# Kernel optimization log

Measured on AMD Instinct MI355X. Metric: run time of the kernel, lower is better.

Reference implementation:

```python
import jax, jax.numpy as jnp
import numpy as np

ALPHA = 4.0          # spikingjelly default surrogate.Sigmoid(alpha=4.0)
V_TH = 1.0           # IFNode default v_threshold
BN_EPS = 1e-5

@jax.custom_vjp
def spike(x):
    # heaviside forward
    return (x >= 0.0).astype(x.dtype)

def _spike_fwd(x):
    return spike(x), x

def _spike_bwd(x, g):
    s = jax.nn.sigmoid(ALPHA * x)
    return (g * ALPHA * s * (1.0 - s),)

spike.defvjp(_spike_fwd, _spike_bwd)

def if_node(x_seq):
    """Multi-step IF neuron: integrate, threshold, hard reset (v_reset=0),
    detach_reset=True. x_seq: [T, ...] -> spikes [T, ...]."""
    def step(v, xt):
        v = v + xt
        s = spike(v - V_TH)
        v = v * (1.0 - jax.lax.stop_gradient(s))  # detached hard reset to 0
        return v, s
    _, s_seq = jax.lax.scan(step, jnp.zeros_like(x_seq[0]), x_seq)
    return s_seq

def bn1d(x, gamma, beta):
    """Training-mode BatchNorm1d over flattened (T*B) batch dim. x: [T,B,F]."""
    m = x.mean(axis=(0, 1))
    v = x.var(axis=(0, 1))  # biased variance, matches torch normalization
    return (x - m) * jax.lax.rsqrt(v + BN_EPS) * gamma + beta

def setup_inputs() -> dict:
    key = jax.random.key(0)
    ks = jax.random.split(key, 12)
    T, B, C, H, W = 8, 64, 2, 128, 128
    F0, D, NC = C * H * W, 2048, 1000
    x = jax.random.uniform(ks[0], (T, B, C, H, W), dtype=jnp.float32)
    def kaiming(k, out_f, in_f):
        # kaiming_normal_ mode='fan_out', relu gain: std = sqrt(2/out_f)
        return jax.random.normal(k, (out_f, in_f), dtype=jnp.float32) * np.sqrt(2.0 / out_f)
    def bias(k, out_f, in_f):
        bound = 1.0 / np.sqrt(in_f)
        return jax.random.uniform(k, (out_f,), dtype=jnp.float32, minval=-bound, maxval=bound)
    inp = {"x": x}
    dims = [(D, F0), (D, D), (D, D)]
    for i, (o, f) in enumerate(dims):
        inp[f"W{i}"] = kaiming(ks[1 + i], o, f)
        inp[f"b{i}"] = bias(ks[4 + i], o, f)
        inp[f"g{i}"] = jnp.ones((o,), jnp.float32)
        inp[f"be{i}"] = jnp.zeros((o,), jnp.float32)
    inp["Wout"] = kaiming(ks[7], NC, D)
    inp["bout"] = bias(ks[8], NC, D)
    return inp

def reference(x, W0, b0, g0, be0, W1, b1, g1, be1, W2, b2, g2, be2, Wout, bout):
    T, B = x.shape[0], x.shape[1]
    h = x.reshape(T, B, -1)           # [T,B,32768]
    h = if_node(h)                    # sn0
    for Wl, bl, gl, bel in ((W0, b0, g0, be0), (W1, b1, g1, be1), (W2, b2, g2, be2)):
        h = jnp.einsum('tbi,oi->tbo', h, Wl) + bl
        h = bn1d(h, gl, bel)
        h = if_node(h)
    out = jnp.einsum('tbi,oi->tbo', h, Wout) + bout  # [T,B,1000]
    return out.mean(axis=0)           # [B,1000]
```

## Files before the change

kernel.cpp:

```cpp
#include <hip/hip_runtime.h>


#define T_STEPS 8
#define BATCH 64
#define F0 32768
#define DIM 2048
#define NROWS 512
#define NC 1000

typedef __attribute__((ext_vector_type(8))) short short8;
typedef __attribute__((ext_vector_type(4))) float f32x4;

__device__ __forceinline__ unsigned short bf16_rne(float f) {
    unsigned int u = __float_as_uint(f);
    u += 0x7FFFu + ((u >> 16) & 1u);
    return (unsigned short)(u >> 16);
}

#define BM 128
#define BN 128
#define BK 64

__device__ __forceinline__ short8 lds_frag(const unsigned short* base, int row, int kb) {
    const int off = row * 128 + (kb ^ ((row & 7) << 4));
    return *(const short8*)((const char*)base + off);
}

__global__ __launch_bounds__(256) void gemm_splitk(
    const unsigned short* __restrict__ A, const float* __restrict__ W,
    float* __restrict__ part, int M, int N, int K, int Kpart, int Wrows)
{
    __shared__ unsigned short As[BM * BK];
    __shared__ unsigned short Hs[BN * BK];
    __shared__ unsigned short Ls[BN * BK];

    const int gx = gridDim.x, gy = gridDim.y;
    const int nwg = gx * gy * gridDim.z;
    const int lid = blockIdx.x + gx * (blockIdx.y + gy * blockIdx.z);
    const int cpx = nwg >> 3;
    const int nid = (lid & 7) * cpx + (lid >> 3);
    const int bx  = nid % gx;
    const int by  = (nid / gx) % gy;
    const int kz  = nid / (gx * gy);

    const int tid  = threadIdx.x;
    const int lane = tid & 63;
    const int w    = tid >> 6;
    const int bm   = bx * BM;
    const int bn   = by * BN;
    const int ksteps = Kpart / BK;

    const int wm = (w >> 1) * 64;
    const int wn = (w & 1) * 64;

    f32x4 acc[4][4] = {};

    for (int kt = 0; kt < ksteps; ++kt) {
        const int k0 = kz * Kpart + kt * BK;

#pragma unroll
        for (int c = 0; c < 4; ++c) {
            const int r    = w * 32 + c * 8 + (lane >> 3);
            const int colb = ((lane & 7) * 16) ^ ((r & 7) << 4);
            const char* src = (const char*)A + ((size_t)(bm + r) * K + k0) * 2 + colb;
            unsigned short* dst = &As[(w * 32 + c * 8) * BK];
            __builtin_amdgcn_global_load_lds(
                (const __attribute__((address_space(1))) void*)src,
                (__attribute__((address_space(3))) void*)dst, 16, 0, 0);
        }

        float4 wv[8];
#pragma unroll
        for (int i = 0; i < 8; ++i) {
            const int q  = tid + 256 * i;
            const int n  = q >> 4;
            const int c4 = q & 15;
            const int gn = min(bn + n, Wrows - 1);
            wv[i] = *(const float4*)&W[(size_t)gn * K + k0 + c4 * 4];
        }
#pragma unroll
        for (int i = 0; i < 8; ++i) {
            const int q  = tid + 256 * i;
            const int n  = q >> 4;
            const int c4 = q & 15;
            const float vf[4] = {wv[i].x, wv[i].y, wv[i].z, wv[i].w};
            unsigned short h[4], l[4];
#pragma unroll
            for (int e = 0; e < 4; ++e) {
                h[e] = bf16_rne(vf[e]);
                const float hf = __uint_as_float((unsigned int)h[e] << 16);
                l[e] = bf16_rne(vf[e] - hf);
            }
            const int off = n * 128 + (((c4 * 8)) ^ ((n & 7) << 4));
            *(ushort4*)((char*)Hs + off) = make_ushort4(h[0], h[1], h[2], h[3]);
            *(ushort4*)((char*)Ls + off) = make_ushort4(l[0], l[1], l[2], l[3]);
        }

        __syncthreads();

#pragma unroll
        for (int kk = 0; kk < 2; ++kk) {
            const int kb = (kk * 32 + (lane >> 4) * 8) * 2;
            short8 a[4], bh[4], bl[4];
#pragma unroll
            for (int i = 0; i < 4; ++i)
                a[i] = lds_frag(As, wm + i * 16 + (lane & 15), kb);
#pragma unroll
            for (int i = 0; i < 4; ++i) {
                const int r = wn + i * 16 + (lane & 15);
                bh[i] = lds_frag(Hs, r, kb);
                bl[i] = lds_frag(Ls, r, kb);
            }
#pragma unroll
            for (int mi = 0; mi < 4; ++mi)
#pragma unroll
                for (int ni = 0; ni < 4; ++ni) {
                    acc[mi][ni] = __builtin_amdgcn_mfma_f32_16x16x32_bf16(
                        a[mi], bh[ni], acc[mi][ni], 0, 0, 0);
                    acc[mi][ni] = __builtin_amdgcn_mfma_f32_16x16x32_bf16(
                        a[mi], bl[ni], acc[mi][ni], 0, 0, 0);
                }
        }
        __syncthreads();
    }

    const size_t zoff = (size_t)kz * M * N;
#pragma unroll
    for (int mi = 0; mi < 4; ++mi) {
        const int gr0 = bm + wm + mi * 16 + (lane >> 4) * 4;
#pragma unroll
        for (int ni = 0; ni < 4; ++ni) {
            const int gc = bn + wn + ni * 16 + (lane & 15);
            if (gc < N) {
#pragma unroll
                for (int e = 0; e < 4; ++e) {
                    const int gr = gr0 + e;
                    if (gr < M) part[zoff + (size_t)gr * N + gc] = acc[mi][ni][e];
                }
            }
        }
    }
}

__global__ __launch_bounds__(256) void reduce_bias(
    const float* __restrict__ part, const float* __restrict__ bias,
    float* __restrict__ out, int KS, int MN, int N)
{
    const int i4 = blockIdx.x * 256 + threadIdx.x;
    if (i4 * 4 >= MN) return;
    float4 s = make_float4(0.f, 0.f, 0.f, 0.f);
    for (int z = 0; z < KS; ++z) {
        const float4 p = *(const float4*)&part[(size_t)z * MN + i4 * 4];
        s.x += p.x; s.y += p.y; s.z += p.z; s.w += p.w;
    }
    const int col = (i4 * 4) % N;
    const float4 b = *(const float4*)&bias[col];
    s.x += b.x; s.y += b.y; s.z += b.z; s.w += b.w;
    *(float4*)&out[(size_t)i4 * 4] = s;
}

__global__ __launch_bounds__(256) void if0_kernel(
    const float* __restrict__ x, unsigned short* __restrict__ s)
{
    const size_t id = (size_t)blockIdx.x * blockDim.x + threadIdx.x;
    float v = 0.f;
#pragma unroll
    for (int t = 0; t < T_STEPS; ++t) {
        const size_t idx = (size_t)t * (BATCH * (size_t)F0) + id;
        v += x[idx];
        if (v >= 1.0f) { s[idx] = 0x3F80; v = 0.f; }
        else           { s[idx] = 0; }
    }
}

__global__ __launch_bounds__(256) void bn_stats(
    const float* __restrict__ z, const float* __restrict__ g,
    const float* __restrict__ be, float* __restrict__ scale,
    float* __restrict__ shift)
{
    __shared__ float ssum[4][64], ssq[4][64];
    const int l = threadIdx.x & 63;
    const int q = threadIdx.x >> 6;
    const int f = blockIdx.x * 64 + l;
    float sum = 0.f, sq = 0.f;
    for (int r = q; r < NROWS; r += 4) {
        const float v = z[(size_t)r * DIM + f];
        sum += v; sq += v * v;
    }
    ssum[q][l] = sum; ssq[q][l] = sq;
    __syncthreads();
    if (threadIdx.x < 64) {
        float ts = 0.f, tq = 0.f;
#pragma unroll
        for (int i = 0; i < 4; ++i) { ts += ssum[i][l]; tq += ssq[i][l]; }
        const float mean = ts * (1.0f / NROWS);
        const float var  = tq * (1.0f / NROWS) - mean * mean;
        const float inv  = rsqrtf(var + 1e-5f);
        const float sc   = g[f] * inv;
        scale[f] = sc;
        shift[f] = be[f] - mean * sc;
    }
}

__global__ __launch_bounds__(256) void bn_if(
    const float* __restrict__ z, const float* __restrict__ scale,
    const float* __restrict__ shift, unsigned short* __restrict__ s)
{
    const int id = blockIdx.x * blockDim.x + threadIdx.x;
    const int o  = id & (DIM - 1);
    const float sc = scale[o];
    const float sh = shift[o];
    float v = 0.f;
#pragma unroll
    for (int t = 0; t < T_STEPS; ++t) {
        const size_t idx = (size_t)t * (BATCH * DIM) + id;
        v += z[idx] * sc + sh;
        if (v >= 1.0f) { s[idx] = 0x3F80; v = 0.f; }
        else           { s[idx] = 0; }
    }
}

__global__ __launch_bounds__(256) void bn_if_mean(
    const float* __restrict__ z, const float* __restrict__ scale,
    const float* __restrict__ shift, unsigned short* __restrict__ sbar)
{
    const int id = blockIdx.x * blockDim.x + threadIdx.x;
    const int o  = id & (DIM - 1);
    const float sc = scale[o];
    const float sh = shift[o];
    float v = 0.f;
    int cnt = 0;
#pragma unroll
    for (int t = 0; t < T_STEPS; ++t) {
        const size_t idx = (size_t)t * (BATCH * DIM) + id;
        v += z[idx] * sc + sh;
        if (v >= 1.0f) { cnt++; v = 0.f; }
    }
    sbar[id] = bf16_rne((float)cnt * 0.125f);
}

extern "C" void kernel_launch(void* const* d_in, const int* in_sizes, int n_in,
                              void* d_out, int out_size, void* d_ws, size_t ws_size,
                              hipStream_t stream)
{
    const float* x    = (const float*)d_in[0];
    const float* W0   = (const float*)d_in[1];
    const float* b0   = (const float*)d_in[2];
    const float* g0   = (const float*)d_in[3];
    const float* be0  = (const float*)d_in[4];
    const float* W1   = (const float*)d_in[5];
    const float* b1   = (const float*)d_in[6];
    const float* g1   = (const float*)d_in[7];
    const float* be1  = (const float*)d_in[8];
    const float* W2   = (const float*)d_in[9];
    const float* b2   = (const float*)d_in[10];
    const float* g2   = (const float*)d_in[11];
    const float* be2  = (const float*)d_in[12];
    const float* Wout = (const float*)d_in[13];
    const float* bout = (const float*)d_in[14];
    float* out = (float*)d_out;
    (void)in_sizes; (void)n_in; (void)out_size; (void)ws_size;

    char* ws = (char*)d_ws;
    size_t off = 0;
    auto alloc = [&](size_t nbytes) {
        char* p = ws + off;
        off = (off + nbytes + 255) & ~(size_t)255;
        return p;
    };
    unsigned short* s0 = (unsigned short*)alloc((size_t)NROWS * F0 * 2);
    unsigned short* s1 = (unsigned short*)alloc((size_t)NROWS * DIM * 2);
    unsigned short* s2 = (unsigned short*)alloc((size_t)NROWS * DIM * 2);
    unsigned short* sb = (unsigned short*)alloc((size_t)128 * DIM * 2);
    float* z    = (float*)alloc((size_t)NROWS * DIM * 4);
    float* part = (float*)alloc((size_t)16 * NROWS * DIM * 4);
    float* scale = (float*)alloc(DIM * 4);
    float* shift = (float*)alloc(DIM * 4);

    const int MN = NROWS * DIM;

    if0_kernel<<<(BATCH * (size_t)F0) / 256, 256, 0, stream>>>(x, s0);

    gemm_splitk<<<dim3(NROWS / BM, DIM / BN, 16), 256, 0, stream>>>(
        s0, W0, part, NROWS, DIM, F0, F0 / 16, DIM);
    reduce_bias<<<MN / 4 / 256, 256, 0, stream>>>(part, b0, z, 16, MN, DIM);
    bn_stats<<<DIM / 64, 256, 0, stream>>>(z, g0, be0, scale, shift);
    bn_if<<<(BATCH * DIM) / 256, 256, 0, stream>>>(z, scale, shift, s1);

    gemm_splitk<<<dim3(NROWS / BM, DIM / BN, 8), 256, 0, stream>>>(
        s1, W1, part, NROWS, DIM, DIM, DIM / 8, DIM);
    reduce_bias<<<MN / 4 / 256, 256, 0, stream>>>(part, b1, z, 8, MN, DIM);
    bn_stats<<<DIM / 64, 256, 0, stream>>>(z, g1, be1, scale, shift);
    bn_if<<<(BATCH * DIM) / 256, 256, 0, stream>>>(z, scale, shift, s2);

    gemm_splitk<<<dim3(NROWS / BM, DIM / BN, 8), 256, 0, stream>>>(
        s2, W2, part, NROWS, DIM, DIM, DIM / 8, DIM);
    reduce_bias<<<MN / 4 / 256, 256, 0, stream>>>(part, b2, z, 8, MN, DIM);
    bn_stats<<<DIM / 64, 256, 0, stream>>>(z, g2, be2, scale, shift);
    bn_if_mean<<<(BATCH * DIM) / 256, 256, 0, stream>>>(z, scale, shift, sb);

    gemm_splitk<<<dim3(1, (NC + BN - 1) / BN, 4), 256, 0, stream>>>(
        sb, Wout, part, BATCH, NC, DIM, DIM / 4, NC);
    reduce_bias<<<(BATCH * NC / 4 + 255) / 256, 256, 0, stream>>>(
        part, bout, out, 4, BATCH * NC, NC);
}
```

Baseline: 408.4 us.

## Double-buffer GEMM with direct fp32 weight LDS loads and fuse BN stats with IF

The split-K GEMM now double-buffers its tiles with BK 32. It stages both the spike activations and the raw fp32 weights into LDS through async global_load_lds, and does the bf16 hi/lo split at fragment-load time instead of during staging. This is meant to overlap global loads with MFMA work and drop the register round-trip for weights. The cost is that each wave now repeats the hi/lo conversion for its fragments. Separately, the BN-stats and IF/mean kernels are fused into one launch per layer, so the scale/shift buffers and extra launches go away, but only 32 blocks now do the IF pass.

Result: slower. 482.8 us (+18.2%).

```diff
diff --git a/kernel.cpp b/kernel.cpp
--- a/kernel.cpp
+++ b/kernel.cpp
@@ -19,20 +19,14 @@
 
 #define BM 128
 #define BN 128
-#define BK 64
-
-__device__ __forceinline__ short8 lds_frag(const unsigned short* base, int row, int kb) {
-    const int off = row * 128 + (kb ^ ((row & 7) << 4));
-    return *(const short8*)((const char*)base + off);
-}
+#define BK 32
 
 __global__ __launch_bounds__(256) void gemm_splitk(
     const unsigned short* __restrict__ A, const float* __restrict__ W,
     float* __restrict__ part, int M, int N, int K, int Kpart, int Wrows)
 {
-    __shared__ unsigned short As[BM * BK];
-    __shared__ unsigned short Hs[BN * BK];
-    __shared__ unsigned short Ls[BN * BK];
+    __shared__ unsigned short As[2][BM * BK];
+    __shared__ float          Wf[2][BN * BK];
 
     const int gx = gridDim.x, gy = gridDim.y;
     const int nwg = gx * gy * gridDim.z;
@@ -49,79 +43,78 @@
     const int bm   = bx * BM;
     const int bn   = by * BN;
     const int ksteps = Kpart / BK;
-
     const int wm = (w >> 1) * 64;
     const int wn = (w & 1) * 64;
 
+    const int aslot = ((lane & 3) ^ ((lane >> 3) & 3)) << 4;
+    const int wslot = ((lane & 7) ^ (lane >> 3)) << 4;
+    const int arow  = w * 32 + (lane >> 2);
+    const int wrow  = w * 32 + (lane >> 3);
+    const size_t abase = (size_t)(bm + arow) * K;
+    const int kbase = kz * Kpart;
+
     f32x4 acc[4][4] = {};
 
-    for (int kt = 0; kt < ksteps; ++kt) {
-        const int k0 = kz * Kpart + kt * BK;
-
-#pragma unroll
-        for (int c = 0; c < 4; ++c) {
-            const int r    = w * 32 + c * 8 + (lane >> 3);
-            const int colb = ((lane & 7) * 16) ^ ((r & 7) << 4);
-            const char* src = (const char*)A + ((size_t)(bm + r) * K + k0) * 2 + colb;
-            unsigned short* dst = &As[(w * 32 + c * 8) * BK];
+    auto stage = [&](int buf, int kt) {
+        const int k0 = kbase + kt * BK;
+#pragma unroll
+        for (int c = 0; c < 2; ++c) {
+            const char* src = (const char*)A + (abase + (size_t)c * 16 * K + k0) * 2 + aslot;
             __builtin_amdgcn_global_load_lds(
                 (const __attribute__((address_space(1))) void*)src,
-                (__attribute__((address_space(3))) void*)dst, 16, 0, 0);
-        }
-
-        float4 wv[8];
-#pragma unroll
-        for (int i = 0; i < 8; ++i) {
-            const int q  = tid + 256 * i;
-            const int n  = q >> 4;
-            const int c4 = q & 15;
-            const int gn = min(bn + n, Wrows - 1);
-            wv[i] = *(const float4*)&W[(size_t)gn * K + k0 + c4 * 4];
-        }
-#pragma unroll
-        for (int i = 0; i < 8; ++i) {
-            const int q  = tid + 256 * i;
-            const int n  = q >> 4;
-            const int c4 = q & 15;
-            const float vf[4] = {wv[i].x, wv[i].y, wv[i].z, wv[i].w};
-            unsigned short h[4], l[4];
-#pragma unroll
-            for (int e = 0; e < 4; ++e) {
-                h[e] = bf16_rne(vf[e]);
-                const float hf = __uint_as_float((unsigned int)h[e] << 16);
-                l[e] = bf16_rne(vf[e] - hf);
+                (__attribute__((address_space(3))) void*)&As[buf][(w * 32 + c * 16) * BK],
+                16, 0, 0);
+        }
+#pragma unroll
+        for (int c = 0; c < 4; ++c) {
+            const int rg = min(bn + wrow + c * 8, Wrows - 1);
+            const char* src = (const char*)W + ((size_t)rg * K + k0) * 4 + wslot;
+            __builtin_amdgcn_global_load_lds(
+                (const __attribute__((address_space(1))) void*)src,
+                (__attribute__((address_space(3))) void*)&Wf[buf][(w * 32 + c * 8) * BK],
+                16, 0, 0);
+        }
+    };
+
+    stage(0, 0);
+    __syncthreads();
+
+    const int aphys = (((lane >> 4)) ^ ((lane >> 1) & 3)) << 4;
+    const int ws0   = (((lane >> 4) * 2)     ^ (lane & 7)) << 4;
+    const int ws1   = (((lane >> 4) * 2 + 1) ^ (lane & 7)) << 4;
+
+    int cur = 0;
+    for (int kt = 0; kt < ksteps; ++kt) {
+        if (kt + 1 < ksteps) stage(cur ^ 1, kt + 1);
+
+        short8 a[4];
+#pragma unroll
+        for (int mi = 0; mi < 4; ++mi) {
+            const int ra = wm + mi * 16 + (lane & 15);
+            a[mi] = *(const short8*)((const char*)As[cur] + ra * 64 + aphys);
+        }
+#pragma unroll
+        for (int ni = 0; ni < 4; ++ni) {
+            const int rw = wn + ni * 16 + (lane & 15);
+            const char* rowp = (const char*)Wf[cur] + rw * 128;
+            const float4 w0 = *(const float4*)(rowp + ws0);
+            const float4 w1 = *(const float4*)(rowp + ws1);
+            const float vf[8] = {w0.x, w0.y, w0.z, w0.w, w1.x, w1.y, w1.z, w1.w};
+            short8 bh, bl;
+#pragma unroll
+            for (int e = 0; e < 8; ++e) {
+                const unsigned short h = bf16_rne(vf[e]);
+                bh[e] = (short)h;
+                bl[e] = (short)bf16_rne(vf[e] - __uint_as_float((unsigned int)h << 16));
             }
-            const int off = n * 128 + (((c4 * 8)) ^ ((n & 7) << 4));
-            *(ushort4*)((char*)Hs + off) = make_ushort4(h[0], h[1], h[2], h[3]);
-            *(ushort4*)((char*)Ls + off) = make_ushort4(l[0], l[1], l[2], l[3]);
-        }
-
+#pragma unroll
+            for (int mi = 0; mi < 4; ++mi) {
+                acc[mi][ni] = __builtin_amdgcn_mfma_f32_16x16x32_bf16(a[mi], bh, acc[mi][ni], 0, 0, 0);
+                acc[mi][ni] = __builtin_amdgcn_mfma_f32_16x16x32_bf16(a[mi], bl, acc[mi][ni], 0, 0, 0);
+            }
+        }
         __syncthreads();
-
-#pragma unroll
-        for (int kk = 0; kk < 2; ++kk) {
-            const int kb = (kk * 32 + (lane >> 4) * 8) * 2;
-            short8 a[4], bh[4], bl[4];
-#pragma unroll
-            for (int i = 0; i < 4; ++i)
-                a[i] = lds_frag(As, wm + i * 16 + (lane & 15), kb);
-#pragma unroll
-            for (int i = 0; i < 4; ++i) {
-                const int r = wn + i * 16 + (lane & 15);
-                bh[i] = lds_frag(Hs, r, kb);
-                bl[i] = lds_frag(Ls, r, kb);
-            }
-#pragma unroll
-            for (int mi = 0; mi < 4; ++mi)
-#pragma unroll
-                for (int ni = 0; ni < 4; ++ni) {
-                    acc[mi][ni] = __builtin_amdgcn_mfma_f32_16x16x32_bf16(
-                        a[mi], bh[ni], acc[mi][ni], 0, 0, 0);
-                    acc[mi][ni] = __builtin_amdgcn_mfma_f32_16x16x32_bf16(
-                        a[mi], bl[ni], acc[mi][ni], 0, 0, 0);
-                }
-        }
-        __syncthreads();
+        cur ^= 1;
     }
 
     const size_t zoff = (size_t)kz * M * N;
@@ -173,12 +166,12 @@
     }
 }
 
-__global__ __launch_bounds__(256) void bn_stats(
+__global__ __launch_bounds__(256) void bn_stats_if(
     const float* __restrict__ z, const float* __restrict__ g,
-    const float* __restrict__ be, float* __restrict__ scale,
-    float* __restrict__ shift)
+    const float* __restrict__ be, unsigned short* __restrict__ s)
 {
     __shared__ float ssum[4][64], ssq[4][64];
+    __shared__ float ssc[64], ssh[64];
     const int l = threadIdx.x & 63;
     const int q = threadIdx.x >> 6;
     const int f = blockIdx.x * 64 + l;
@@ -197,46 +190,67 @@
         const float var  = tq * (1.0f / NROWS) - mean * mean;
         const float inv  = rsqrtf(var + 1e-5f);
         const float sc   = g[f] * inv;
-        scale[f] = sc;
-        shift[f] = be[f] - mean * sc;
-    }
-}
-
-__global__ __launch_bounds__(256) void bn_if(
-    const float* __restrict__ z, const float* __restrict__ scale,
-    const float* __restrict__ shift, unsigned short* __restrict__ s)
-{
-    const int id = blockIdx.x * blockDim.x + threadIdx.x;
-    const int o  = id & (DIM - 1);
-    const float sc = scale[o];
-    const float sh = shift[o];
-    float v = 0.f;
-#pragma unroll
-    for (int t = 0; t < T_STEPS; ++t) {
-        const size_t idx = (size_t)t * (BATCH * DIM) + id;
-        v += z[idx] * sc + sh;
-        if (v >= 1.0f) { s[idx] = 0x3F80; v = 0.f; }
-        else           { s[idx] = 0; }
-    }
-}
-
-__global__ __launch_bounds__(256) void bn_if_mean(
-    const float* __restrict__ z, const float* __restrict__ scale,
-    const float* __restrict__ shift, unsigned short* __restrict__ sbar)
-{
-    const int id = blockIdx.x * blockDim.x + threadIdx.x;
-    const int o  = id & (DIM - 1);
-    const float sc = scale[o];
-    const float sh = shift[o];
-    float v = 0.f;
-    int cnt = 0;
-#pragma unroll
-    for (int t = 0; t < T_STEPS; ++t) {
-        const size_t idx = (size_t)t * (BATCH * DIM) + id;
-        v += z[idx] * sc + sh;
-        if (v >= 1.0f) { cnt++; v = 0.f; }
-    }
-    sbar[id] = bf16_rne((float)cnt * 0.125f);
+        ssc[l] = sc;
+        ssh[l] = be[f] - mean * sc;
+    }
+    __syncthreads();
+    const float sc = ssc[l];
+    const float sh = ssh[l];
+    for (int b = q; b < BATCH; b += 4) {
+        const int id = b * DIM + f;
+        float v = 0.f;
+#pragma unroll
+        for (int t = 0; t < T_STEPS; ++t) {
+            const size_t idx = (size_t)t * (BATCH * DIM) + id;
+            v += z[idx] * sc + sh;
+            if (v >= 1.0f) { s[idx] = 0x3F80; v = 0.f; }
+            else           { s[idx] = 0; }
+        }
+    }
+}
+
+__global__ __launch_bounds__(256) void bn_stats_if_mean(
+    const float* __restrict__ z, const float* __restrict__ g,
+    const float* __restrict__ be, unsigned short* __restrict__ sbar)
+{
+    __shared__ float ssum[4][64], ssq[4][64];
+    __shared__ float ssc[64], ssh[64];
+    const int l = threadIdx.x & 63;
+    const int q = threadIdx.x >> 6;
+    const int f = blockIdx.x * 64 + l;
+    float sum = 0.f, sq = 0.f;
+    for (int r = q; r < NROWS; r += 4) {
+        const float v = z[(size_t)r * DIM + f];
+        sum += v; sq += v * v;
+    }
+    ssum[q][l] = sum; ssq[q][l] = sq;
+    __syncthreads();
+    if (threadIdx.x < 64) {
+        float ts = 0.f, tq = 0.f;
+#pragma unroll
+        for (int i = 0; i < 4; ++i) { ts += ssum[i][l]; tq += ssq[i][l]; }
+        const float mean = ts * (1.0f / NROWS);
+        const float var  = tq * (1.0f / NROWS) - mean * mean;
+        const float inv  = rsqrtf(var + 1e-5f);
+        const float sc   = g[f] * inv;
+        ssc[l] = sc;
+        ssh[l] = be[f] - mean * sc;
+    }
+    __syncthreads();
+    const float sc = ssc[l];
+    const float sh = ssh[l];
+    for (int b = q; b < BATCH; b += 4) {
+        const int id = b * DIM + f;
+        float v = 0.f;
+        int cnt = 0;
+#pragma unroll
+        for (int t = 0; t < T_STEPS; ++t) {
+            const size_t idx = (size_t)t * (BATCH * DIM) + id;
+            v += z[idx] * sc + sh;
+            if (v >= 1.0f) { cnt++; v = 0.f; }
+        }
+        sbar[id] = bf16_rne((float)cnt * 0.125f);
+    }
 }
 
 extern "C" void kernel_launch(void* const* d_in, const int* in_sizes, int n_in,
@@ -274,8 +288,6 @@
     unsigned short* sb = (unsigned short*)alloc((size_t)128 * DIM * 2);
     float* z    = (float*)alloc((size_t)NROWS * DIM * 4);
     float* part = (float*)alloc((size_t)16 * NROWS * DIM * 4);
-    float* scale = (float*)alloc(DIM * 4);
-    float* shift = (float*)alloc(DIM * 4);
 
     const int MN = NROWS * DIM;
 
@@ -284,20 +296,17 @@
     gemm_splitk<<<dim3(NROWS / BM, DIM / BN, 16), 256, 0, stream>>>(
         s0, W0, part, NROWS, DIM, F0, F0 / 16, DIM);
     reduce_bias<<<MN / 4 / 256, 256, 0, stream>>>(part, b0, z, 16, MN, DIM);
-    bn_stats<<<DIM / 64, 256, 0, stream>>>(z, g0, be0, scale, shift);
-    bn_if<<<(BATCH * DIM) / 256, 256, 0, stream>>>(z, scale, shift, s1);
+    bn_stats_if<<<DIM / 64, 256, 0, stream>>>(z, g0, be0, s1);
 
     gemm_splitk<<<dim3(NROWS / BM, DIM / BN, 8), 256, 0, stream>>>(
         s1, W1, part, NROWS, DIM, DIM, DIM / 8, DIM);
     reduce_bias<<<MN / 4 / 256, 256, 0, stream>>>(part, b1, z, 8, MN, DIM);
-    bn_stats<<<DIM / 64, 256, 0, stream>>>(z, g1, be1, scale, shift);
-    bn_if<<<(BATCH * DIM) / 256, 256, 0, stream>>>(z, scale, shift, s2);
+    bn_stats_if<<<DIM / 64, 256, 0, stream>>>(z, g1, be1, s2);
 
     gemm_splitk<<<dim3(NROWS / BM, DIM / BN, 8), 256, 0, stream>>>(
         s2, W2, part, NROWS, DIM, DIM, DIM / 8, DIM);
     reduce_bias<<<MN / 4 / 256, 256, 0, stream>>>(part, b2, z, 8, MN, DIM);
-    bn_stats<<<DIM / 64, 256, 0, stream>>>(z, g2, be2, scale, shift);
-    bn_if_mean<<<(BATCH * DIM) / 256, 256, 0, stream>>>(z, scale, shift, sb);
+    bn_stats_if_mean<<<DIM / 64, 256, 0, stream>>>(z, g2, be2, sb);
 
     gemm_splitk<<<dim3(1, (NC + BN - 1) / BN, 4), 256, 0, stream>>>(
         sb, Wout, part, BATCH, NC, DIM, DIM / 4, NC);
```
